# Performance work log

Hardware: AMD Instinct MI355X
Metric: run time of the kernel (lower is better)

The kernel has to match this reference:

```python
import jax, jax.numpy as jnp
import numpy as np

N_NODES = 100000
N_EDGES = 1600000
VOCAB = 2048
NODE_DIM = 64
HIDDEN = 64
N_MASK = 10000


def setup_inputs() -> dict:
    key = jax.random.key(0)
    ks = jax.random.split(key, 10)
    x = jax.random.randint(ks[0], (N_NODES, 1), 0, VOCAB, dtype=jnp.int64)
    edge_index = jax.random.randint(ks[1], (2, N_EDGES), 0, N_NODES, dtype=jnp.int64)
    mask_x_position = jax.random.randint(ks[2], (N_MASK,), 0, N_NODES, dtype=jnp.int64)
    # embedding init: normal with std = node_dim ** -0.5 (as in initialize_parameters)
    emb = jax.random.normal(ks[3], (VOCAB, NODE_DIM), dtype=jnp.float32) * (NODE_DIM ** -0.5)
    # SAGEConv layer 1: lin_l (neighbors, with bias), lin_r (root, no bias)
    s1 = (NODE_DIM ** -0.5)
    W_l1 = jax.random.uniform(ks[4], (NODE_DIM, HIDDEN), jnp.float32, -s1, s1)
    b_l1 = jnp.zeros((HIDDEN,), jnp.float32)
    W_r1 = jax.random.uniform(ks[5], (NODE_DIM, HIDDEN), jnp.float32, -s1, s1)
    # SAGEConv layer 2
    s2 = (HIDDEN ** -0.5)
    W_l2 = jax.random.uniform(ks[6], (HIDDEN, VOCAB), jnp.float32, -s2, s2)
    b_l2 = jnp.zeros((VOCAB,), jnp.float32)
    W_r2 = jax.random.uniform(ks[7], (HIDDEN, VOCAB), jnp.float32, -s2, s2)
    return {"x": x, "edge_index": edge_index, "mask_x_position": mask_x_position,
            "emb": emb, "W_l1": W_l1, "b_l1": b_l1, "W_r1": W_r1,
            "W_l2": W_l2, "b_l2": b_l2, "W_r2": W_r2}


def _sage_conv(h, src, dst, W_l, b_l, W_r):
    # mean-aggregate source-node features at destination nodes (PyG SAGEConv, aggr='mean')
    msgs = h[src]                                                  # [E, D]
    agg = jax.ops.segment_sum(msgs, dst, num_segments=N_NODES)     # [N, D]
    deg = jax.ops.segment_sum(jnp.ones((src.shape[0], 1), h.dtype), dst,
                              num_segments=N_NODES)                # [N, 1]
    mean = agg / jnp.maximum(deg, 1.0)
    return mean @ W_l + b_l + h @ W_r


def reference(x, edge_index, mask_x_position, emb, W_l1, b_l1, W_r1, W_l2, b_l2, W_r2):
    src, dst = edge_index[0], edge_index[1]
    h = emb[x[:, 0]]                                # embedding(x).squeeze(1) -> [N, node_dim]
    # dropout is identity in eval mode
    h = _sage_conv(h, src, dst, W_l1, b_l1, W_r1)   # [N, hidden]
    h = jax.nn.relu(h)
    h = _sage_conv(h, src, dst, W_l2, b_l2, W_r2)   # [N, vocab]
    return jax.nn.log_softmax(h[mask_x_position], axis=1)
```

## Files before the change

kernel.cpp:

```cpp
#include <hip/hip_runtime.h>
#include <math.h>

#define N_NODES   100000
#define N_EDGES   1600000
#define VOCAB     2048
#define NODE_DIM  64
#define HIDDEN    64
#define N_MASK    10000

#define BN        192
#define NBKT      521
#define CHUNK     2048
#define NCH       782
#define ELCAP     4096

typedef __attribute__((ext_vector_type(8))) short short8;
typedef __attribute__((ext_vector_type(4))) float f32x4;
typedef unsigned short ushort_t;
typedef unsigned int uint_t;

#define H1_OFF      0
#define ESRC_OFF    25600000
#define E2_OFF      32000000
#define EWL_OFF     44800000
#define EWR_OFF     45324288
#define W2T_OFF     45848576
#define X2B_OFF     46372864
#define ROWPTR_OFF  48932864
#define BCNT_OFF    49332880
#define BPTR_OFF    49334976
#define MAT_OFF     49337072

__device__ __forceinline__ ushort_t f2bf(float f) {
    uint_t u = __builtin_bit_cast(uint_t, f);
    u += 0x7FFFu + ((u >> 16) & 1u);
    return (ushort_t)(u >> 16);
}

__global__ __launch_bounds__(256) void k_prep(const float* __restrict__ emb,
                                              const float* __restrict__ Wl1,
                                              const float* __restrict__ Wr1,
                                              const float* __restrict__ Wl2,
                                              const float* __restrict__ Wr2,
                                              float* __restrict__ embWl,
                                              float* __restrict__ embWr,
                                              ushort_t* __restrict__ W2T) {
    __shared__ ushort_t T[64 * 66];
    const int bx = blockIdx.x;
    const int tid = threadIdx.x;
    if (bx < 1024) {
        const int half = bx >> 9;
        const float* W = half ? Wr1 : Wl1;
        float* out = half ? embWr : embWl;
        int idx = (bx & 511) * 256 + tid;
        int v = idx >> 6, c = idx & 63;
        float s = 0.0f;
#pragma unroll 8
        for (int k = 0; k < 64; k++) s += emb[v * 64 + k] * W[k * 64 + c];
        out[idx] = s;
    } else {
        int t = bx - 1024;
        const int k0 = (t & 1) * 64;
        const int n0 = (t >> 1) * 64;
        const float* Wsrc = (k0 == 0) ? Wl2 : Wr2;
#pragma unroll
        for (int i = 0; i < 16; i++) {
            int idx = i * 256 + tid;
            int k = idx >> 6, n = idx & 63;
            T[n * 66 + k] = f2bf(Wsrc[(size_t)k * VOCAB + n0 + n]);
        }
        __syncthreads();
#pragma unroll
        for (int i = 0; i < 16; i++) {
            int idx = i * 256 + tid;
            int n = idx >> 6, k = idx & 63;
            W2T[(size_t)(n0 + n) * 128 + k0 + k] = T[n * 66 + k];
        }
    }
}

__global__ __launch_bounds__(256) void k_count2(const int* __restrict__ dst,
                                                int* __restrict__ mat) {
    __shared__ int hist[NBKT];
    const int c = blockIdx.x, t = threadIdx.x;
    const int e0 = c * CHUNK;
    const int n = min(CHUNK, N_EDGES - e0);
    for (int i = t; i < NBKT; i += 256) hist[i] = 0;
    int d[8];
#pragma unroll
    for (int i = 0; i < 8; i++) {
        int idx = i * 256 + t;
        d[i] = (idx < n) ? dst[e0 + idx] : -1;
    }
    __syncthreads();
#pragma unroll
    for (int i = 0; i < 8; i++)
        if (d[i] >= 0) atomicAdd(&hist[d[i] / BN], 1);
    __syncthreads();
    for (int i = t; i < NBKT; i += 256) mat[(size_t)c * NBKT + i] = hist[i];
}

__global__ __launch_bounds__(1024) void k_mscan(int* __restrict__ mat,
                                                int* __restrict__ bcnt) {
    __shared__ int s[1024];
    const int b = blockIdx.x, t = threadIdx.x;
    int v = (t < NCH) ? mat[(size_t)t * NBKT + b] : 0;
    s[t] = v;
    __syncthreads();
    for (int off = 1; off < 1024; off <<= 1) {
        int a = (t >= off) ? s[t - off] : 0;
        __syncthreads();
        s[t] += a;
        __syncthreads();
    }
    if (t < NCH) mat[(size_t)t * NBKT + b] = s[t] - v;
    if (t == NCH - 1) bcnt[b] = s[t];
}

__global__ __launch_bounds__(1024) void k_bscan(const int* __restrict__ bcnt,
                                                int* __restrict__ bptr,
                                                int* __restrict__ rowptr) {
    __shared__ int s[1024];
    int t = threadIdx.x;
    int v = (t < NBKT) ? bcnt[t] : 0;
    s[t] = v;
    __syncthreads();
    for (int off = 1; off < 1024; off <<= 1) {
        int a = (t >= off) ? s[t - off] : 0;
        __syncthreads();
        s[t] += a;
        __syncthreads();
    }
    if (t < NBKT) bptr[t] = s[t] - v;
    if (t == NBKT - 1) bptr[NBKT] = s[t];
    if (t == 0) rowptr[N_NODES] = N_EDGES;
}

__global__ __launch_bounds__(256) void k_scatter3(const int* __restrict__ src,
                                                  const int* __restrict__ dst,
                                                  const int* __restrict__ x,
                                                  const int* __restrict__ mat,
                                                  const int* __restrict__ bptr,
                                                  int2* __restrict__ e2) {
    __shared__ int cur[NBKT];
    const int c = blockIdx.x, t = threadIdx.x;
    const int e0 = c * CHUNK;
    const int n = min(CHUNK, N_EDGES - e0);
    for (int i = t; i < NBKT; i += 256)
        cur[i] = bptr[i] + mat[(size_t)c * NBKT + i];
    int d[8], sv[8], voc[8];
#pragma unroll
    for (int i = 0; i < 8; i++) {
        int idx = i * 256 + t;
        if (idx < n) { d[i] = dst[e0 + idx]; sv[i] = src[e0 + idx]; }
        else d[i] = -1;
    }
#pragma unroll
    for (int i = 0; i < 8; i++)
        if (d[i] >= 0) voc[i] = x[sv[i]];
    __syncthreads();
#pragma unroll
    for (int i = 0; i < 8; i++) {
        if (d[i] >= 0) {
            int b = d[i] / BN;
            int pos = atomicAdd(&cur[b], 1);
            e2[pos] = make_int2(sv[i], (voc[i] << 8) | (d[i] - b * BN));
        }
    }
}

__global__ __launch_bounds__(512) void k_sortagg(const int* __restrict__ bptr,
                                                 const int2* __restrict__ e2,
                                                 const int* __restrict__ x,
                                                 const float* __restrict__ embWl,
                                                 const float* __restrict__ embWr,
                                                 const float* __restrict__ b1,
                                                 int* __restrict__ rowptr,
                                                 int* __restrict__ esrc,
                                                 float* __restrict__ h1) {
    __shared__ int2 eL[ELCAP];
    __shared__ int sc[256];
    __shared__ int cur[BN];
    __shared__ int base[BN + 1];
    const int b = blockIdx.x;
    const int t = threadIdx.x;
    const int r0 = bptr[b], r1 = bptr[b + 1];
    const int m = r1 - r0;

    if (t < 256) sc[t] = 0;
    __syncthreads();
    for (int i = t; i < m; i += 512)
        atomicAdd(&sc[e2[r0 + i].y & 255], 1);
    __syncthreads();
    int v = (t < 256) ? sc[t] : 0;
    for (int off = 1; off < 256; off <<= 1) {
        int a = (t >= off && t < 256) ? sc[t - off] : 0;
        __syncthreads();
        if (t < 256) sc[t] += a;
        __syncthreads();
    }
    if (t < BN) {
        int excl = sc[t] - v;
        base[t] = excl;
        cur[t] = excl;
        int node = b * BN + t;
        if (node < N_NODES) rowptr[node] = r0 + excl;
        if (t == BN - 1) base[BN] = sc[t];
    }
    __syncthreads();
    for (int i = t; i < m; i += 512) {
        int2 ev = e2[r0 + i];
        int pos = atomicAdd(&cur[ev.y & 255], 1);
        eL[pos] = ev;
    }
    __syncthreads();
    for (int i = t; i < m; i += 512)
        esrc[r0 + i] = eL[i].x;

    const int wv = t >> 6, lane = t & 63;
    const float b1v = b1[lane];
    for (int nl = wv; nl < BN; nl += 8) {
        int node = b * BN + nl;
        if (node >= N_NODES) break;
        int j0 = base[nl], j1 = base[nl + 1];
        int deg = j1 - j0;
        float s0 = 0.0f, s1 = 0.0f, s2 = 0.0f, s3 = 0.0f;
        int j = j0;
        for (; j + 3 < j1; j += 4) {
            int va = eL[j].y >> 8;
            int vb = eL[j + 1].y >> 8;
            int vc = eL[j + 2].y >> 8;
            int vd = eL[j + 3].y >> 8;
            s0 += embWl[(va << 6) + lane];
            s1 += embWl[(vb << 6) + lane];
            s2 += embWl[(vc << 6) + lane];
            s3 += embWl[(vd << 6) + lane];
        }
        for (; j < j1; j++)
            s0 += embWl[((eL[j].y >> 8) << 6) + lane];
        float sum = (s0 + s1) + (s2 + s3);
        float inv = 1.0f / fmaxf((float)deg, 1.0f);
        float self = embWr[(x[node] << 6) + lane];
        h1[((size_t)node << 6) + lane] = fmaxf(sum * inv + self + b1v, 0.0f);
    }
}

__global__ __launch_bounds__(256) void k_x2(const int* __restrict__ mask,
                                            const int* __restrict__ rowptr,
                                            const int* __restrict__ esrc,
                                            const float* __restrict__ h1,
                                            ushort_t* __restrict__ X2b) {
    int gw = (blockIdx.x * 256 + threadIdx.x) >> 6;
    int lane = threadIdx.x & 63;
    if (gw >= N_MASK) return;
    int n = mask[gw];
    int r0 = rowptr[n], r1 = rowptr[n + 1];
    int deg = r1 - r0;
    float s0 = 0.0f, s1 = 0.0f, s2 = 0.0f, s3 = 0.0f;
    for (int base = 0; base < deg; base += 64) {
        int cnt = min(64, deg - base);
        int mys = (base + lane < deg) ? esrc[r0 + base + lane] : 0;
        int t = 0;
        for (; t + 3 < cnt; t += 4) {
            int sa = __shfl(mys, t);
            int sb = __shfl(mys, t + 1);
            int sc = __shfl(mys, t + 2);
            int sd = __shfl(mys, t + 3);
            s0 += h1[((size_t)sa << 6) + lane];
            s1 += h1[((size_t)sb << 6) + lane];
            s2 += h1[((size_t)sc << 6) + lane];
            s3 += h1[((size_t)sd << 6) + lane];
        }
        for (; t < cnt; t++)
            s0 += h1[((size_t)__shfl(mys, t) << 6) + lane];
    }
    float sum = (s0 + s1) + (s2 + s3);
    float inv = 1.0f / fmaxf((float)deg, 1.0f);
    X2b[gw * 128 + lane]      = f2bf(sum * inv);
    X2b[gw * 128 + 64 + lane] = f2bf(h1[((size_t)n << 6) + lane]);
}

__global__ __launch_bounds__(256) void k_gemm2_mfma(const ushort_t* __restrict__ X2b,
                                                    const ushort_t* __restrict__ W2T,
                                                    const float* __restrict__ bias,
                                                    float* __restrict__ out,
                                                    int M) {
    __shared__ ushort_t As[64 * 144];
    __shared__ ushort_t Bs[64 * 144];
    const int tid  = threadIdx.x;
    const int row0 = blockIdx.x * 64;
    const int col0 = blockIdx.y * 64;

#pragma unroll
    for (int i = 0; i < 4; i++) {
        int idx = i * 256 + tid;
        int r = idx >> 4, ch = idx & 15;
        int R = row0 + r;
        short8 v = {0, 0, 0, 0, 0, 0, 0, 0};
        if (R < M) v = *(const short8*)(X2b + (size_t)R * 128 + ch * 8);
        *(short8*)(As + r * 144 + ch * 8) = v;
    }
#pragma unroll
    for (int i = 0; i < 4; i++) {
        int idx = i * 256 + tid;
        int r = idx >> 4, ch = idx & 15;
        *(short8*)(Bs + r * 144 + ch * 8) =
            *(const short8*)(W2T + (size_t)(col0 + r) * 128 + ch * 8);
    }
    __syncthreads();

    const int lane = tid & 63;
    const int wv   = tid >> 6;
    const int wr = wv >> 1, wc = wv & 1;
    const int l15 = lane & 15, q = lane >> 4;

    f32x4 acc[2][2] = {};
    const ushort_t* Abase = As + (wr * 32 + l15) * 144 + q * 8;
    const ushort_t* Bbase = Bs + (wc * 32 + l15) * 144 + q * 8;

#pragma unroll
    for (int ks = 0; ks < 4; ks++) {
        short8 a0 = *(const short8*)(Abase + ks * 32);
        short8 a1 = *(const short8*)(Abase + 16 * 144 + ks * 32);
        short8 b0 = *(const short8*)(Bbase + ks * 32);
        short8 b1 = *(const short8*)(Bbase + 16 * 144 + ks * 32);
        acc[0][0] = __builtin_amdgcn_mfma_f32_16x16x32_bf16(a0, b0, acc[0][0], 0, 0, 0);
        acc[0][1] = __builtin_amdgcn_mfma_f32_16x16x32_bf16(a0, b1, acc[0][1], 0, 0, 0);
        acc[1][0] = __builtin_amdgcn_mfma_f32_16x16x32_bf16(a1, b0, acc[1][0], 0, 0, 0);
        acc[1][1] = __builtin_amdgcn_mfma_f32_16x16x32_bf16(a1, b1, acc[1][1], 0, 0, 0);
    }

#pragma unroll
    for (int ni = 0; ni < 2; ni++) {
        int c_ = col0 + wc * 32 + ni * 16 + l15;
        float bv = bias[c_];
#pragma unroll
        for (int mi = 0; mi < 2; mi++) {
#pragma unroll
            for (int reg = 0; reg < 4; reg++) {
                int r_ = row0 + wr * 32 + mi * 16 + q * 4 + reg;
                if (r_ < M) out[(size_t)r_ * VOCAB + c_] = acc[mi][ni][reg] + bv;
            }
        }
    }
}

__global__ __launch_bounds__(256) void k_logsoftmax(float* __restrict__ out) {
    const int row = blockIdx.x;
    float4* p4 = (float4*)(out + (size_t)row * VOCAB);
    const int tid = threadIdx.x;
    float4 v[2];
    float m = -INFINITY;
#pragma unroll
    for (int i = 0; i < 2; i++) {
        v[i] = p4[tid + i * 256];
        m = fmaxf(m, fmaxf(fmaxf(v[i].x, v[i].y), fmaxf(v[i].z, v[i].w)));
    }
#pragma unroll
    for (int off = 1; off < 64; off <<= 1) m = fmaxf(m, __shfl_xor(m, off));
    __shared__ float redm[4];
    __shared__ float reds[4];
    int wave = tid >> 6;
    if ((tid & 63) == 0) redm[wave] = m;
    __syncthreads();
    m = fmaxf(fmaxf(redm[0], redm[1]), fmaxf(redm[2], redm[3]));
    float s = 0.0f;
#pragma unroll
    for (int i = 0; i < 2; i++)
        s += expf(v[i].x - m) + expf(v[i].y - m) + expf(v[i].z - m) + expf(v[i].w - m);
#pragma unroll
    for (int off = 1; off < 64; off <<= 1) s += __shfl_xor(s, off);
    if ((tid & 63) == 0) reds[wave] = s;
    __syncthreads();
    s = reds[0] + reds[1] + reds[2] + reds[3];
    float L = m + logf(s);
#pragma unroll
    for (int i = 0; i < 2; i++) {
        float4 o = v[i];
        o.x -= L; o.y -= L; o.z -= L; o.w -= L;
        p4[tid + i * 256] = o;
    }
}

extern "C" void kernel_launch(void* const* d_in, const int* in_sizes, int n_in,
                              void* d_out, int out_size, void* d_ws, size_t ws_size,
                              hipStream_t stream) {
    const int*   x    = (const int*)d_in[0];
    const int*   ei   = (const int*)d_in[1];
    const int*   src  = ei;
    const int*   dst  = ei + N_EDGES;
    const int*   mask = (const int*)d_in[2];
    const float* emb  = (const float*)d_in[3];
    const float* Wl1  = (const float*)d_in[4];
    const float* bl1  = (const float*)d_in[5];
    const float* Wr1  = (const float*)d_in[6];
    const float* Wl2  = (const float*)d_in[7];
    const float* bl2  = (const float*)d_in[8];
    const float* Wr2  = (const float*)d_in[9];
    float* out = (float*)d_out;

    char* ws = (char*)d_ws;
    float*    h1     = (float*)(ws + H1_OFF);
    int*      esrc   = (int*)(ws + ESRC_OFF);
    int2*     e2     = (int2*)(ws + E2_OFF);
    float*    embWl  = (float*)(ws + EWL_OFF);
    float*    embWr  = (float*)(ws + EWR_OFF);
    ushort_t* W2T    = (ushort_t*)(ws + W2T_OFF);
    ushort_t* X2b    = (ushort_t*)(ws + X2B_OFF);
    int*      rowptr = (int*)(ws + ROWPTR_OFF);
    int*      bcnt   = (int*)(ws + BCNT_OFF);
    int*      bptr   = (int*)(ws + BPTR_OFF);
    int*      mat    = (int*)(ws + MAT_OFF);

    k_count2  <<<NCH, 256, 0, stream>>>(dst, mat);
    k_mscan   <<<NBKT, 1024, 0, stream>>>(mat, bcnt);
    k_bscan   <<<1, 1024, 0, stream>>>(bcnt, bptr, rowptr);
    k_scatter3<<<NCH, 256, 0, stream>>>(src, dst, x, mat, bptr, e2);

    k_prep<<<1088, 256, 0, stream>>>(emb, Wl1, Wr1, Wl2, Wr2, embWl, embWr, W2T);

    k_sortagg<<<NBKT, 512, 0, stream>>>(bptr, e2, x, embWl, embWr, bl1, rowptr, esrc, h1);

    k_x2<<<(N_MASK * 64 + 255) / 256, 256, 0, stream>>>(mask, rowptr, esrc, h1, X2b);
    dim3 g2((N_MASK + 63) / 64, VOCAB / 64);
    k_gemm2_mfma<<<g2, 256, 0, stream>>>(X2b, W2T, bl2, out, N_MASK);

    k_logsoftmax<<<N_MASK, 256, 0, stream>>>(out);
}
```

Baseline: 267.1 us.

## Halve destination bucket size and store per-chunk histogram matrix as ushort

Node bucket size drops from 192 to 96, which doubles the bucket count to 1042. k_sortagg therefore gets twice as many blocks with half the shared-memory edge list, aiming at better occupancy and parallelism on the GPU. The per-chunk bucket count matrix is stored as 16-bit values to cut its memory traffic. The bucket scan now handles two buckets per thread so it fits 1024 threads. The risk is more scan and histogram work, plus a 16-bit overflow if one chunk-bucket offset ever exceeds 65535.

New measurement: 264.0 us. Within noise of the previous version (-1.2%).

```diff
diff --git a/kernel.cpp b/kernel.cpp
--- a/kernel.cpp
+++ b/kernel.cpp
@@ -8,11 +8,11 @@
 #define HIDDEN    64
 #define N_MASK    10000
 
-#define BN        192
-#define NBKT      521
+#define BN        96
+#define NBKT      1042
 #define CHUNK     2048
 #define NCH       782
-#define ELCAP     4096
+#define ELCAP     2048
 
 typedef __attribute__((ext_vector_type(8))) short short8;
 typedef __attribute__((ext_vector_type(4))) float f32x4;
@@ -28,8 +28,8 @@
 #define X2B_OFF     46372864
 #define ROWPTR_OFF  48932864
 #define BCNT_OFF    49332880
-#define BPTR_OFF    49334976
-#define MAT_OFF     49337072
+#define BPTR_OFF    49337056
+#define MAT_OFF     49341232
 
 __device__ __forceinline__ ushort_t f2bf(float f) {
     uint_t u = __builtin_bit_cast(uint_t, f);
@@ -80,7 +80,7 @@
 }
 
 __global__ __launch_bounds__(256) void k_count2(const int* __restrict__ dst,
-                                                int* __restrict__ mat) {
+                                                ushort_t* __restrict__ mat) {
     __shared__ int hist[NBKT];
     const int c = blockIdx.x, t = threadIdx.x;
     const int e0 = c * CHUNK;
@@ -97,14 +97,14 @@
     for (int i = 0; i < 8; i++)
         if (d[i] >= 0) atomicAdd(&hist[d[i] / BN], 1);
     __syncthreads();
-    for (int i = t; i < NBKT; i += 256) mat[(size_t)c * NBKT + i] = hist[i];
-}
-
-__global__ __launch_bounds__(1024) void k_mscan(int* __restrict__ mat,
+    for (int i = t; i < NBKT; i += 256) mat[(size_t)c * NBKT + i] = (ushort_t)hist[i];
+}
+
+__global__ __launch_bounds__(1024) void k_mscan(ushort_t* __restrict__ mat,
                                                 int* __restrict__ bcnt) {
     __shared__ int s[1024];
     const int b = blockIdx.x, t = threadIdx.x;
-    int v = (t < NCH) ? mat[(size_t)t * NBKT + b] : 0;
+    int v = (t < NCH) ? (int)mat[(size_t)t * NBKT + b] : 0;
     s[t] = v;
     __syncthreads();
     for (int off = 1; off < 1024; off <<= 1) {
@@ -113,7 +113,7 @@
         s[t] += a;
         __syncthreads();
     }
-    if (t < NCH) mat[(size_t)t * NBKT + b] = s[t] - v;
+    if (t < NCH) mat[(size_t)t * NBKT + b] = (ushort_t)(s[t] - v);
     if (t == NCH - 1) bcnt[b] = s[t];
 }
 
@@ -122,24 +122,29 @@
                                                 int* __restrict__ rowptr) {
     __shared__ int s[1024];
     int t = threadIdx.x;
-    int v = (t < NBKT) ? bcnt[t] : 0;
+    int i0 = 2 * t, i1 = 2 * t + 1;
+    int a = (i0 < NBKT) ? bcnt[i0] : 0;
+    int b = (i1 < NBKT) ? bcnt[i1] : 0;
+    int v = a + b;
     s[t] = v;
     __syncthreads();
     for (int off = 1; off < 1024; off <<= 1) {
-        int a = (t >= off) ? s[t - off] : 0;
-        __syncthreads();
-        s[t] += a;
-        __syncthreads();
-    }
-    if (t < NBKT) bptr[t] = s[t] - v;
-    if (t == NBKT - 1) bptr[NBKT] = s[t];
+        int p = (t >= off) ? s[t - off] : 0;
+        __syncthreads();
+        s[t] += p;
+        __syncthreads();
+    }
+    int excl = s[t] - v;
+    if (i0 < NBKT) bptr[i0] = excl;
+    if (i1 < NBKT) bptr[i1] = excl + a;
+    if (t == 1023) bptr[NBKT] = s[t];
     if (t == 0) rowptr[N_NODES] = N_EDGES;
 }
 
 __global__ __launch_bounds__(256) void k_scatter3(const int* __restrict__ src,
                                                   const int* __restrict__ dst,
                                                   const int* __restrict__ x,
-                                                  const int* __restrict__ mat,
+                                                  const ushort_t* __restrict__ mat,
                                                   const int* __restrict__ bptr,
                                                   int2* __restrict__ e2) {
     __shared__ int cur[NBKT];
@@ -147,7 +152,7 @@
     const int e0 = c * CHUNK;
     const int n = min(CHUNK, N_EDGES - e0);
     for (int i = t; i < NBKT; i += 256)
-        cur[i] = bptr[i] + mat[(size_t)c * NBKT + i];
+        cur[i] = bptr[i] + (int)mat[(size_t)c * NBKT + i];
     int d[8], sv[8], voc[8];
 #pragma unroll
     for (int i = 0; i < 8; i++) {
@@ -179,7 +184,7 @@
                                                  int* __restrict__ esrc,
                                                  float* __restrict__ h1) {
     __shared__ int2 eL[ELCAP];
-    __shared__ int sc[256];
+    __shared__ int sc[128];
     __shared__ int cur[BN];
     __shared__ int base[BN + 1];
     const int b = blockIdx.x;
@@ -187,16 +192,16 @@
     const int r0 = bptr[b], r1 = bptr[b + 1];
     const int m = r1 - r0;
 
-    if (t < 256) sc[t] = 0;
+    if (t < 128) sc[t] = 0;
     __syncthreads();
     for (int i = t; i < m; i += 512)
         atomicAdd(&sc[e2[r0 + i].y & 255], 1);
     __syncthreads();
-    int v = (t < 256) ? sc[t] : 0;
-    for (int off = 1; off < 256; off <<= 1) {
-        int a = (t >= off && t < 256) ? sc[t - off] : 0;
-        __syncthreads();
-        if (t < 256) sc[t] += a;
+    int v = (t < 128) ? sc[t] : 0;
+    for (int off = 1; off < 128; off <<= 1) {
+        int a = (t >= off && t < 128) ? sc[t - off] : 0;
+        __syncthreads();
+        if (t < 128) sc[t] += a;
         __syncthreads();
     }
     if (t < BN) {
@@ -410,7 +415,7 @@
     int*      rowptr = (int*)(ws + ROWPTR_OFF);
     int*      bcnt   = (int*)(ws + BCNT_OFF);
     int*      bptr   = (int*)(ws + BPTR_OFF);
-    int*      mat    = (int*)(ws + MAT_OFF);
+    ushort_t* mat    = (ushort_t*)(ws + MAT_OFF);
 
     k_count2  <<<NCH, 256, 0, stream>>>(dst, mat);
     k_mscan   <<<NBKT, 1024, 0, stream>>>(mat, bcnt);
```
